# Kernel tuning notes

Hardware: AMD Instinct MI355X
Metric: run time of the kernel (lower is better)

The kernel has to match this reference:

```python
import jax, jax.numpy as jnp
import numpy as np

# Config constants (match init_kwargs)
THR = 0.2
TEMPERATURE = 0.1
BORDER_RM = 2
H0C, W0C = 60, 80  # L = 4800
H1C, W1C = 60, 80  # S = 4800


def setup_inputs() -> dict:
    key = jax.random.key(0)
    k0, k1 = jax.random.split(key)
    feat_c0 = jax.random.normal(k0, (2, 4800, 256), dtype=jnp.float32)
    feat_c1 = jax.random.normal(k1, (2, 4800, 256), dtype=jnp.float32)
    return {"feat_c0": feat_c0, "feat_c1": feat_c1}


def _border_mask_1d(h, w, b):
    """Flattened [h*w] bool mask that is False within b of any border."""
    ih = jnp.arange(h)
    iw = jnp.arange(w)
    mh = (ih >= b) & (ih < h - b)
    mw = (iw >= b) & (iw < w - b)
    return (mh[:, None] & mw[None, :]).reshape(-1)


def reference(feat_c0, feat_c1):
    N, L, C = feat_c0.shape
    # Normalize features and compute similarity (dual-softmax)
    scale = 1.0 / (C ** 0.5)
    sim = jnp.einsum('nlc,nsc->nls', feat_c0 * scale, feat_c1 * scale) / TEMPERATURE
    conf = jax.nn.softmax(sim, axis=1) * jax.nn.softmax(sim, axis=2)  # [N, L, S]

    # Threshold + border removal (mask_border path, no padding masks)
    bm0 = _border_mask_1d(H0C, W0C, BORDER_RM)  # [L]
    bm1 = _border_mask_1d(H1C, W1C, BORDER_RM)  # [S]
    mask = (conf > THR) & bm0[None, :, None] & bm1[None, None, :]

    # Mutual nearest neighbor
    mask = mask \
        & (conf == jnp.max(conf, axis=2, keepdims=True)) \
        & (conf == jnp.max(conf, axis=1, keepdims=True))

    # Per-row match: j index of the (at most one) surviving entry, and its conf.
    # Fixed-shape analogue of torch.where extraction: mconf==0 means no match.
    mask_v = jnp.any(mask, axis=2)                         # [N, L]
    j_ids = jnp.argmax(mask, axis=2)                       # [N, L]
    mconf = jnp.take_along_axis(conf, j_ids[..., None], axis=2)[..., 0]
    mconf = jnp.where(mask_v, mconf, 0.0)                  # [N, L]

    return conf, mask_v, j_ids, mconf
```

## Files before the change

kernel.cpp:

```cpp
#include <hip/hip_runtime.h>
#include <hip/hip_bf16.h>
#include <cstdint>

#define L_DIM 4800
#define C_DIM 256
#define CONF_ELEMS ((size_t)2 * L_DIM * L_DIM)

typedef _Float16 f16x8 __attribute__((ext_vector_type(8)));
typedef float f32x4 __attribute__((ext_vector_type(4)));

typedef const __attribute__((address_space(1))) uint32_t glb_u32;
typedef __attribute__((address_space(3))) uint32_t lds_u32;

#define WS_F16_NEEDED 15705600

__global__ __launch_bounds__(256) void k_cvt2(const float* __restrict__ f0,
                                              const float* __restrict__ f1,
                                              _Float16* __restrict__ h0,
                                              _Float16* __restrict__ h1) {
    int b = blockIdx.x;
    const float* src = (b < 1200) ? f0 : f1;
    _Float16* dst = (b < 1200) ? h0 : h1;
    int i = (b < 1200 ? b : b - 1200) * 256 + threadIdx.x;
    const float4* s4 = (const float4*)src;
    float4 a = s4[(size_t)i * 2], c = s4[(size_t)i * 2 + 1];
    f16x8 h = { (_Float16)a.x, (_Float16)a.y, (_Float16)a.z, (_Float16)a.w,
                (_Float16)c.x, (_Float16)c.y, (_Float16)c.z, (_Float16)c.w };
    *(f16x8*)(dst + (size_t)i * 8) = h;
}

__global__ __launch_bounds__(256) void k_reduceA(const float* __restrict__ partA,
                                                 float* __restrict__ invsum) {
    int i = blockIdx.x * 256 + threadIdx.x;
    if (i >= 19200) return;
    int base = (i < 9600) ? 0 : 50;
    int j = (i < 9600) ? i : i - 9600;
    float s = 0.f;
#pragma unroll 10
    for (int k = 0; k < 50; ++k)
        s += partA[(size_t)(base + k) * 9600 + j];
    invsum[i] = 1.0f / s;
}

__global__ __launch_bounds__(256) void k_reduceB(const unsigned* __restrict__ colbest,
                                                 unsigned* __restrict__ colmaxF) {
    int i = blockIdx.x * 256 + threadIdx.x;
    if (i >= 9600) return;
    unsigned m = 0u;
#pragma unroll 10
    for (int k = 0; k < 50; ++k)
        m = max(m, colbest[(size_t)k * 9600 + i]);
    colmaxF[i] = m;
}

template<bool F16SRC, bool FINAL>
__global__ __launch_bounds__(256) void k_gemm2(const void* __restrict__ srcA,
                                               const void* __restrict__ srcB,
                                               float* __restrict__ conf,
                                               const float* __restrict__ invsum,
                                               float* __restrict__ partA,
                                               unsigned long long* __restrict__ rowbest,
                                               unsigned* __restrict__ colbest) {
    const int xcd = blockIdx.x & 7;
    const int idx = blockIdx.x >> 3;
    const int t   = xcd * 625 + idx;
    const int n   = t / 2500;
    const int rem = t - n * 2500;
    const int ty  = rem / 50;
    const int tx  = rem - ty * 50;
    const int l0  = ty * 96;
    const int s0  = tx * 96;

    __shared__ __align__(16) _Float16 As[96 * 64];
    __shared__ __align__(16) _Float16 Bs[96 * 64];
    __shared__ __align__(16) char redbuf[2304];

    const int tid  = threadIdx.x;
    const int lane = tid & 63;
    const int w    = tid >> 6;
    const int wr   = w >> 1, wc = w & 1;
    const int q    = lane >> 4, r16 = lane & 15;

    f32x4 acc[3][3] = {};

    for (int kt = 0; kt < 4; ++kt) {
        const int k0 = kt * 64;
        __syncthreads();
        if constexpr (F16SRC) {
            const _Float16* A = (const _Float16*)srcA + ((size_t)n * L_DIM + l0) * C_DIM;
            const _Float16* B = (const _Float16*)srcB + ((size_t)n * L_DIM + s0) * C_DIM;
#pragma unroll
            for (int i = 0; i < 3; ++i) {
                int c   = tid + i * 256;
                int row = c >> 3;
                int kc  = (c & 7) ^ (row & 7);
                __builtin_amdgcn_global_load_lds(
                    (glb_u32*)(A + (size_t)row * C_DIM + k0 + kc * 8),
                    (lds_u32*)(As + (i * 256 + w * 64) * 8), 16, 0, 0);
                __builtin_amdgcn_global_load_lds(
                    (glb_u32*)(B + (size_t)row * C_DIM + k0 + kc * 8),
                    (lds_u32*)(Bs + (i * 256 + w * 64) * 8), 16, 0, 0);
            }
        } else {
            const float* A = (const float*)srcA + ((size_t)n * L_DIM + l0) * C_DIM;
            const float* B = (const float*)srcB + ((size_t)n * L_DIM + s0) * C_DIM;
#pragma unroll
            for (int i = 0; i < 3; ++i) {
                int c   = tid + i * 256;
                int row = c >> 3;
                int kc  = (c & 7) ^ (row & 7);
                const float* pa = A + (size_t)row * C_DIM + k0 + kc * 8;
                const float* pb = B + (size_t)row * C_DIM + k0 + kc * 8;
                float4 a0 = ((const float4*)pa)[0], a1 = ((const float4*)pa)[1];
                float4 b0 = ((const float4*)pb)[0], b1 = ((const float4*)pb)[1];
                f16x8 ha = { (_Float16)a0.x, (_Float16)a0.y, (_Float16)a0.z, (_Float16)a0.w,
                             (_Float16)a1.x, (_Float16)a1.y, (_Float16)a1.z, (_Float16)a1.w };
                f16x8 hb = { (_Float16)b0.x, (_Float16)b0.y, (_Float16)b0.z, (_Float16)b0.w,
                             (_Float16)b1.x, (_Float16)b1.y, (_Float16)b1.z, (_Float16)b1.w };
                *(f16x8*)(As + (size_t)c * 8) = ha;
                *(f16x8*)(Bs + (size_t)c * 8) = hb;
            }
        }
        __syncthreads();

        f16x8 af[2][3], bf[2][3];
#pragma unroll
        for (int m = 0; m < 3; ++m) {
            int row = wr * 48 + m * 16 + r16;
#pragma unroll
            for (int ks = 0; ks < 2; ++ks)
                af[ks][m] = *(const f16x8*)(As + row * 64 + (((ks * 4 + q) ^ (row & 7)) * 8));
        }
#pragma unroll
        for (int nn = 0; nn < 3; ++nn) {
            int row = wc * 48 + nn * 16 + r16;
#pragma unroll
            for (int ks = 0; ks < 2; ++ks)
                bf[ks][nn] = *(const f16x8*)(Bs + row * 64 + (((ks * 4 + q) ^ (row & 7)) * 8));
        }
#pragma unroll
        for (int ks = 0; ks < 2; ++ks)
#pragma unroll
            for (int m = 0; m < 3; ++m)
#pragma unroll
                for (int nn = 0; nn < 3; ++nn)
                    acc[m][nn] = __builtin_amdgcn_mfma_f32_16x16x32_f16(af[ks][m], bf[ks][nn], acc[m][nn], 0, 0, 0);
    }

    const float SIM_SCALE = 0.0390625f;

    if constexpr (!FINAL) {
        float* redR = (float*)redbuf;
        float* redC = (float*)(redbuf + 768);
        float cp[3] = {0.f, 0.f, 0.f};
#pragma unroll
        for (int m = 0; m < 3; ++m) {
#pragma unroll
            for (int reg = 0; reg < 4; ++reg) {
                float rsum = 0.f;
#pragma unroll
                for (int nn = 0; nn < 3; ++nn) {
                    float e = __expf(acc[m][nn][reg] * SIM_SCALE);
                    rsum += e;
                    cp[nn] += e;
                }
                rsum += __shfl_xor(rsum, 1);
                rsum += __shfl_xor(rsum, 2);
                rsum += __shfl_xor(rsum, 4);
                rsum += __shfl_xor(rsum, 8);
                if (r16 == 0)
                    redR[wc * 96 + wr * 48 + m * 16 + q * 4 + reg] = rsum;
            }
        }
#pragma unroll
        for (int nn = 0; nn < 3; ++nn) {
            float v = cp[nn];
            v += __shfl_xor(v, 16);
            v += __shfl_xor(v, 32);
            if (q == 0)
                redC[wr * 96 + wc * 48 + nn * 16 + r16] = v;
        }
        __syncthreads();
        if (tid < 96) {
            partA[(size_t)tx * 9600 + n * L_DIM + l0 + tid] = redR[tid] + redR[96 + tid];
        } else if (tid < 192) {
            int c = tid - 96;
            partA[(size_t)(50 + ty) * 9600 + n * L_DIM + s0 + c] = redC[c] + redC[96 + c];
        }
    } else {
        unsigned long long* redRB = (unsigned long long*)redbuf;
        unsigned* redCB = (unsigned*)(redbuf + 1536);
        const size_t base = (size_t)n * L_DIM * L_DIM;
        float ivC[3];
#pragma unroll
        for (int nn = 0; nn < 3; ++nn)
            ivC[nn] = invsum[9600 + n * L_DIM + s0 + wc * 48 + nn * 16 + r16];
        float cmx[3] = {0.f, 0.f, 0.f};
#pragma unroll
        for (int m = 0; m < 3; ++m) {
#pragma unroll
            for (int reg = 0; reg < 4; ++reg) {
                const int grow = l0 + wr * 48 + m * 16 + q * 4 + reg;
                const float ivR = invsum[n * L_DIM + grow];
                const size_t rowoff = base + (size_t)grow * L_DIM;
                float bv = -1.f; int bc = 0;
#pragma unroll
                for (int nn = 0; nn < 3; ++nn) {
                    const int gcol = s0 + wc * 48 + nn * 16 + r16;
                    float cf = __expf(acc[m][nn][reg] * (2.0f * SIM_SCALE)) * ivR * ivC[nn];
                    conf[rowoff + gcol] = cf;
                    cmx[nn] = fmaxf(cmx[nn], cf);
                    if (cf > bv) { bv = cf; bc = gcol; }
                }
                unsigned long long pack =
                    ((unsigned long long)__float_as_uint(bv) << 32) |
                    (unsigned long long)(0xFFFFFFFFu - (unsigned)bc);
#pragma unroll
                for (int d = 1; d < 16; d <<= 1) {
                    unsigned long long o = __shfl_xor(pack, d);
                    if (o > pack) pack = o;
                }
                if (r16 == 0)
                    redRB[wc * 96 + wr * 48 + m * 16 + q * 4 + reg] = pack;
            }
        }
#pragma unroll
        for (int nn = 0; nn < 3; ++nn) {
            float v = cmx[nn];
            v = fmaxf(v, __shfl_xor(v, 16));
            v = fmaxf(v, __shfl_xor(v, 32));
            if (q == 0)
                redCB[wr * 96 + wc * 48 + nn * 16 + r16] = __float_as_uint(v);
        }
        __syncthreads();
        if (tid < 96) {
            unsigned long long p0 = redRB[tid], p1 = redRB[96 + tid];
            rowbest[(size_t)tx * 9600 + n * L_DIM + l0 + tid] = (p0 > p1) ? p0 : p1;
        } else if (tid < 192) {
            int c = tid - 96;
            colbest[(size_t)ty * 9600 + n * L_DIM + s0 + c] = max(redCB[c], redCB[96 + c]);
        }
    }
}

__global__ __launch_bounds__(256) void k_match(const unsigned long long* __restrict__ rowbest,
                                               const unsigned* __restrict__ colmaxF,
                                               float* __restrict__ out) {
    int i = blockIdx.x * 256 + threadIdx.x;
    if (i >= 2 * L_DIM) return;
    unsigned long long p = 0ull;
#pragma unroll 10
    for (int k = 0; k < 50; ++k) {
        unsigned long long o = rowbest[(size_t)k * 9600 + i];
        if (o > p) p = o;
    }
    int n = i / L_DIM, l = i % L_DIM;
    float v = __uint_as_float((unsigned)(p >> 32));
    int cand = (int)(0xFFFFFFFFu - (unsigned)(p & 0xFFFFFFFFull));
    if (cand < 0 || cand >= L_DIM) cand = 0;
    int h0 = l / 80, w0 = l % 80;
    int h1 = cand / 80, w1 = cand % 80;
    bool bm0 = (h0 >= 2) && (h0 < 58) && (w0 >= 2) && (w0 < 78);
    bool bm1 = (h1 >= 2) && (h1 < 58) && (w1 >= 2) && (w1 < 78);
    float cm = __uint_as_float(colmaxF[n * L_DIM + cand]);
    bool mask = (v > 0.2f) && bm0 && bm1 && (v == cm);
    out[CONF_ELEMS + i]         = mask ? 1.0f : 0.0f;
    out[CONF_ELEMS + 9600 + i]  = mask ? (float)cand : 0.0f;
    out[CONF_ELEMS + 19200 + i] = mask ? v : 0.0f;
}

extern "C" void kernel_launch(void* const* d_in, const int* in_sizes, int n_in,
                              void* d_out, int out_size, void* d_ws, size_t ws_size,
                              hipStream_t stream) {
    const float* f0 = (const float*)d_in[0];
    const float* f1 = (const float*)d_in[1];
    float* out = (float*)d_out;

    float* invsum = (float*)d_ws;
    unsigned* colmaxF = (unsigned*)((char*)d_ws + 76800);
    float* partA = (float*)((char*)d_ws + 115200);
    unsigned long long* rowbest = (unsigned long long*)((char*)d_ws + 115200);
    unsigned* colbest = (unsigned*)((char*)d_ws + 3955200);
    _Float16* h0 = (_Float16*)((char*)d_ws + 5875200);
    _Float16* h1 = h0 + (size_t)2 * L_DIM * C_DIM;

    const bool usef16 = ws_size >= WS_F16_NEEDED;

    if (usef16) {
        k_cvt2<<<dim3(2400), 256, 0, stream>>>(f0, f1, h0, h1);
        k_gemm2<true, false><<<dim3(5000), 256, 0, stream>>>(
            h0, h1, out, invsum, partA, rowbest, colbest);
        k_reduceA<<<dim3(75), 256, 0, stream>>>(partA, invsum);
        k_gemm2<true, true><<<dim3(5000), 256, 0, stream>>>(
            h0, h1, out, invsum, partA, rowbest, colbest);
    } else {
        k_gemm2<false, false><<<dim3(5000), 256, 0, stream>>>(
            f0, f1, out, invsum, partA, rowbest, colbest);
        k_reduceA<<<dim3(75), 256, 0, stream>>>(partA, invsum);
        k_gemm2<false, true><<<dim3(5000), 256, 0, stream>>>(
            f0, f1, out, invsum, partA, rowbest, colbest);
    }
    k_reduceB<<<dim3(38), 256, 0, stream>>>(colbest, colmaxF);
    k_match<<<dim3(38), 256, 0, stream>>>(rowbest, colmaxF, out);
}
```

Before: 132.7 us.

## Double-buffer LDS tiles in dual-softmax GEMM to overlap loads with MFMA

```diff
diff --git a/kernel.cpp b/kernel.cpp
--- a/kernel.cpp
+++ b/kernel.cpp
@@ -71,8 +71,8 @@
     const int l0  = ty * 96;
     const int s0  = tx * 96;
 
-    __shared__ __align__(16) _Float16 As[96 * 64];
-    __shared__ __align__(16) _Float16 Bs[96 * 64];
+    __shared__ __align__(16) _Float16 As[2][96 * 64];
+    __shared__ __align__(16) _Float16 Bs[2][96 * 64];
     __shared__ __align__(16) char redbuf[2304];
 
     const int tid  = threadIdx.x;
@@ -83,60 +83,61 @@
 
     f32x4 acc[3][3] = {};
 
-    for (int kt = 0; kt < 4; ++kt) {
+    const _Float16* Ah = (const _Float16*)srcA + ((size_t)n * L_DIM + l0) * C_DIM;
+    const _Float16* Bh = (const _Float16*)srcB + ((size_t)n * L_DIM + s0) * C_DIM;
+    const float*    Af = (const float*)srcA + ((size_t)n * L_DIM + l0) * C_DIM;
+    const float*    Bf = (const float*)srcB + ((size_t)n * L_DIM + s0) * C_DIM;
+
+    auto stage = [&](int kt, int buf) {
         const int k0 = kt * 64;
-        __syncthreads();
         if constexpr (F16SRC) {
-            const _Float16* A = (const _Float16*)srcA + ((size_t)n * L_DIM + l0) * C_DIM;
-            const _Float16* B = (const _Float16*)srcB + ((size_t)n * L_DIM + s0) * C_DIM;
 #pragma unroll
             for (int i = 0; i < 3; ++i) {
                 int c   = tid + i * 256;
                 int row = c >> 3;
                 int kc  = (c & 7) ^ (row & 7);
                 __builtin_amdgcn_global_load_lds(
-                    (glb_u32*)(A + (size_t)row * C_DIM + k0 + kc * 8),
-                    (lds_u32*)(As + (i * 256 + w * 64) * 8), 16, 0, 0);
+                    (glb_u32*)(Ah + (size_t)row * C_DIM + k0 + kc * 8),
+                    (lds_u32*)(&As[buf][(i * 256 + w * 64) * 8]), 16, 0, 0);
                 __builtin_amdgcn_global_load_lds(
-                    (glb_u32*)(B + (size_t)row * C_DIM + k0 + kc * 8),
-                    (lds_u32*)(Bs + (i * 256 + w * 64) * 8), 16, 0, 0);
+                    (glb_u32*)(Bh + (size_t)row * C_DIM + k0 + kc * 8),
+                    (lds_u32*)(&Bs[buf][(i * 256 + w * 64) * 8]), 16, 0, 0);
             }
         } else {
-            const float* A = (const float*)srcA + ((size_t)n * L_DIM + l0) * C_DIM;
-            const float* B = (const float*)srcB + ((size_t)n * L_DIM + s0) * C_DIM;
 #pragma unroll
             for (int i = 0; i < 3; ++i) {
                 int c   = tid + i * 256;
                 int row = c >> 3;
                 int kc  = (c & 7) ^ (row & 7);
-                const float* pa = A + (size_t)row * C_DIM + k0 + kc * 8;
-                const float* pb = B + (size_t)row * C_DIM + k0 + kc * 8;
+                const float* pa = Af + (size_t)row * C_DIM + k0 + kc * 8;
+                const float* pb = Bf + (size_t)row * C_DIM + k0 + kc * 8;
                 float4 a0 = ((const float4*)pa)[0], a1 = ((const float4*)pa)[1];
                 float4 b0 = ((const float4*)pb)[0], b1 = ((const float4*)pb)[1];
                 f16x8 ha = { (_Float16)a0.x, (_Float16)a0.y, (_Float16)a0.z, (_Float16)a0.w,
                              (_Float16)a1.x, (_Float16)a1.y, (_Float16)a1.z, (_Float16)a1.w };
                 f16x8 hb = { (_Float16)b0.x, (_Float16)b0.y, (_Float16)b0.z, (_Float16)b0.w,
                              (_Float16)b1.x, (_Float16)b1.y, (_Float16)b1.z, (_Float16)b1.w };
-                *(f16x8*)(As + (size_t)c * 8) = ha;
-                *(f16x8*)(Bs + (size_t)c * 8) = hb;
+                *(f16x8*)(&As[buf][(size_t)c * 8]) = ha;
+                *(f16x8*)(&Bs[buf][(size_t)c * 8]) = hb;
             }
         }
-        __syncthreads();
-
+    };
+
+    auto compute = [&](int buf) {
         f16x8 af[2][3], bf[2][3];
 #pragma unroll
         for (int m = 0; m < 3; ++m) {
             int row = wr * 48 + m * 16 + r16;
 #pragma unroll
             for (int ks = 0; ks < 2; ++ks)
-                af[ks][m] = *(const f16x8*)(As + row * 64 + (((ks * 4 + q) ^ (row & 7)) * 8));
+                af[ks][m] = *(const f16x8*)(&As[buf][row * 64 + (((ks * 4 + q) ^ (row & 7)) * 8)]);
         }
 #pragma unroll
         for (int nn = 0; nn < 3; ++nn) {
             int row = wc * 48 + nn * 16 + r16;
 #pragma unroll
             for (int ks = 0; ks < 2; ++ks)
-                bf[ks][nn] = *(const f16x8*)(Bs + row * 64 + (((ks * 4 + q) ^ (row & 7)) * 8));
+                bf[ks][nn] = *(const f16x8*)(&Bs[buf][row * 64 + (((ks * 4 + q) ^ (row & 7)) * 8)]);
         }
 #pragma unroll
         for (int ks = 0; ks < 2; ++ks)
@@ -145,6 +146,15 @@
 #pragma unroll
                 for (int nn = 0; nn < 3; ++nn)
                     acc[m][nn] = __builtin_amdgcn_mfma_f32_16x16x32_f16(af[ks][m], bf[ks][nn], acc[m][nn], 0, 0, 0);
+    };
+
+    stage(0, 0);
+    __syncthreads();
+#pragma unroll
+    for (int kt = 0; kt < 4; ++kt) {
+        if (kt < 3) stage(kt + 1, (kt + 1) & 1);
+        compute(kt & 1);
+        __syncthreads();
     }
 
     const float SIM_SCALE = 0.0390625f;
```

Result: slower. 147.3 us (+11.0%).

## Loop five tiles per block, use nontemporal conf stores, fuse column-max reduce into match

Applied to the files above, without the earlier changes.

```diff
diff --git a/kernel.cpp b/kernel.cpp
--- a/kernel.cpp
+++ b/kernel.cpp
@@ -42,17 +42,6 @@
     invsum[i] = 1.0f / s;
 }
 
-__global__ __launch_bounds__(256) void k_reduceB(const unsigned* __restrict__ colbest,
-                                                 unsigned* __restrict__ colmaxF) {
-    int i = blockIdx.x * 256 + threadIdx.x;
-    if (i >= 9600) return;
-    unsigned m = 0u;
-#pragma unroll 10
-    for (int k = 0; k < 50; ++k)
-        m = max(m, colbest[(size_t)k * 9600 + i]);
-    colmaxF[i] = m;
-}
-
 template<bool F16SRC, bool FINAL>
 __global__ __launch_bounds__(256) void k_gemm2(const void* __restrict__ srcA,
                                                const void* __restrict__ srcB,
@@ -62,14 +51,7 @@
                                                unsigned long long* __restrict__ rowbest,
                                                unsigned* __restrict__ colbest) {
     const int xcd = blockIdx.x & 7;
-    const int idx = blockIdx.x >> 3;
-    const int t   = xcd * 625 + idx;
-    const int n   = t / 2500;
-    const int rem = t - n * 2500;
-    const int ty  = rem / 50;
-    const int tx  = rem - ty * 50;
-    const int l0  = ty * 96;
-    const int s0  = tx * 96;
+    const int j   = blockIdx.x >> 3;
 
     __shared__ __align__(16) _Float16 As[96 * 64];
     __shared__ __align__(16) _Float16 Bs[96 * 64];
@@ -81,170 +63,181 @@
     const int wr   = w >> 1, wc = w & 1;
     const int q    = lane >> 4, r16 = lane & 15;
 
-    f32x4 acc[3][3] = {};
-
-    for (int kt = 0; kt < 4; ++kt) {
-        const int k0 = kt * 64;
-        __syncthreads();
-        if constexpr (F16SRC) {
-            const _Float16* A = (const _Float16*)srcA + ((size_t)n * L_DIM + l0) * C_DIM;
-            const _Float16* B = (const _Float16*)srcB + ((size_t)n * L_DIM + s0) * C_DIM;
-#pragma unroll
-            for (int i = 0; i < 3; ++i) {
-                int c   = tid + i * 256;
-                int row = c >> 3;
-                int kc  = (c & 7) ^ (row & 7);
-                __builtin_amdgcn_global_load_lds(
-                    (glb_u32*)(A + (size_t)row * C_DIM + k0 + kc * 8),
-                    (lds_u32*)(As + (i * 256 + w * 64) * 8), 16, 0, 0);
-                __builtin_amdgcn_global_load_lds(
-                    (glb_u32*)(B + (size_t)row * C_DIM + k0 + kc * 8),
-                    (lds_u32*)(Bs + (i * 256 + w * 64) * 8), 16, 0, 0);
+    const float SIM_SCALE = 0.0390625f;
+
+    for (int s = 0; s < 5; ++s) {
+        const int t   = xcd * 625 + j + s * 125;
+        const int n   = t / 2500;
+        const int rem = t - n * 2500;
+        const int ty  = rem / 50;
+        const int tx  = rem - ty * 50;
+        const int l0  = ty * 96;
+        const int s0  = tx * 96;
+
+        f32x4 acc[3][3] = {};
+
+        const _Float16* Ah = (const _Float16*)srcA + ((size_t)n * L_DIM + l0) * C_DIM;
+        const _Float16* Bh = (const _Float16*)srcB + ((size_t)n * L_DIM + s0) * C_DIM;
+        const float*    Af = (const float*)srcA + ((size_t)n * L_DIM + l0) * C_DIM;
+        const float*    Bf = (const float*)srcB + ((size_t)n * L_DIM + s0) * C_DIM;
+
+        for (int kt = 0; kt < 4; ++kt) {
+            const int k0 = kt * 64;
+            __syncthreads();
+            if constexpr (F16SRC) {
+#pragma unroll
+                for (int i = 0; i < 3; ++i) {
+                    int c   = tid + i * 256;
+                    int row = c >> 3;
+                    int kc  = (c & 7) ^ (row & 7);
+                    __builtin_amdgcn_global_load_lds(
+                        (glb_u32*)(Ah + (size_t)row * C_DIM + k0 + kc * 8),
+                        (lds_u32*)(As + (i * 256 + w * 64) * 8), 16, 0, 0);
+                    __builtin_amdgcn_global_load_lds(
+                        (glb_u32*)(Bh + (size_t)row * C_DIM + k0 + kc * 8),
+                        (lds_u32*)(Bs + (i * 256 + w * 64) * 8), 16, 0, 0);
+                }
+            } else {
+#pragma unroll
+                for (int i = 0; i < 3; ++i) {
+                    int c   = tid + i * 256;
+                    int row = c >> 3;
+                    int kc  = (c & 7) ^ (row & 7);
+                    const float* pa = Af + (size_t)row * C_DIM + k0 + kc * 8;
+                    const float* pb = Bf + (size_t)row * C_DIM + k0 + kc * 8;
+                    float4 a0 = ((const float4*)pa)[0], a1 = ((const float4*)pa)[1];
+                    float4 b0 = ((const float4*)pb)[0], b1 = ((const float4*)pb)[1];
+                    f16x8 ha = { (_Float16)a0.x, (_Float16)a0.y, (_Float16)a0.z, (_Float16)a0.w,
+                                 (_Float16)a1.x, (_Float16)a1.y, (_Float16)a1.z, (_Float16)a1.w };
+                    f16x8 hb = { (_Float16)b0.x, (_Float16)b0.y, (_Float16)b0.z, (_Float16)b0.w,
+                                 (_Float16)b1.x, (_Float16)b1.y, (_Float16)b1.z, (_Float16)b1.w };
+                    *(f16x8*)(As + (size_t)c * 8) = ha;
+                    *(f16x8*)(Bs + (size_t)c * 8) = hb;
+                }
+            }
+            __syncthreads();
+
+            f16x8 af[2][3], bf[2][3];
+#pragma unroll
+            for (int m = 0; m < 3; ++m) {
+                int row = wr * 48 + m * 16 + r16;
+#pragma unroll
+                for (int ks = 0; ks < 2; ++ks)
+                    af[ks][m] = *(const f16x8*)(As + row * 64 + (((ks * 4 + q) ^ (row & 7)) * 8));
+            }
+#pragma unroll
+            for (int nn = 0; nn < 3; ++nn) {
+                int row = wc * 48 + nn * 16 + r16;
+#pragma unroll
+                for (int ks = 0; ks < 2; ++ks)
+                    bf[ks][nn] = *(const f16x8*)(Bs + row * 64 + (((ks * 4 + q) ^ (row & 7)) * 8));
+            }
+#pragma unroll
+            for (int ks = 0; ks < 2; ++ks)
+#pragma unroll
+                for (int m = 0; m < 3; ++m)
+#pragma unroll
+                    for (int nn = 0; nn < 3; ++nn)
+                        acc[m][nn] = __builtin_amdgcn_mfma_f32_16x16x32_f16(af[ks][m], bf[ks][nn], acc[m][nn], 0, 0, 0);
+        }
+
+        if constexpr (!FINAL) {
+            float* redR = (float*)redbuf;
+            float* redC = (float*)(redbuf + 768);
+            float cp[3] = {0.f, 0.f, 0.f};
+#pragma unroll
+            for (int m = 0; m < 3; ++m) {
+#pragma unroll
+                for (int reg = 0; reg < 4; ++reg) {
+                    float rsum = 0.f;
+#pragma unroll
+                    for (int nn = 0; nn < 3; ++nn) {
+                        float e = __expf(acc[m][nn][reg] * SIM_SCALE);
+                        rsum += e;
+                        cp[nn] += e;
+                    }
+                    rsum += __shfl_xor(rsum, 1);
+                    rsum += __shfl_xor(rsum, 2);
+                    rsum += __shfl_xor(rsum, 4);
+                    rsum += __shfl_xor(rsum, 8);
+                    if (r16 == 0)
+                        redR[wc * 96 + wr * 48 + m * 16 + q * 4 + reg] = rsum;
+                }
+            }
+#pragma unroll
+            for (int nn = 0; nn < 3; ++nn) {
+                float v = cp[nn];
+                v += __shfl_xor(v, 16);
+                v += __shfl_xor(v, 32);
+                if (q == 0)
+                    redC[wr * 96 + wc * 48 + nn * 16 + r16] = v;
+            }
+            __syncthreads();
+            if (tid < 96) {
+                partA[(size_t)tx * 9600 + n * L_DIM + l0 + tid] = redR[tid] + redR[96 + tid];
+            } else if (tid < 192) {
+                int c = tid - 96;
+                partA[(size_t)(50 + ty) * 9600 + n * L_DIM + s0 + c] = redC[c] + redC[96 + c];
             }
         } else {
-            const float* A = (const float*)srcA + ((size_t)n * L_DIM + l0) * C_DIM;
-            const float* B = (const float*)srcB + ((size_t)n * L_DIM + s0) * C_DIM;
-#pragma unroll
-            for (int i = 0; i < 3; ++i) {
-                int c   = tid + i * 256;
-                int row = c >> 3;
-                int kc  = (c & 7) ^ (row & 7);
-                const float* pa = A + (size_t)row * C_DIM + k0 + kc * 8;
-                const float* pb = B + (size_t)row * C_DIM + k0 + kc * 8;
-                float4 a0 = ((const float4*)pa)[0], a1 = ((const float4*)pa)[1];
-                float4 b0 = ((const float4*)pb)[0], b1 = ((const float4*)pb)[1];
-                f16x8 ha = { (_Float16)a0.x, (_Float16)a0.y, (_Float16)a0.z, (_Float16)a0.w,
-                             (_Float16)a1.x, (_Float16)a1.y, (_Float16)a1.z, (_Float16)a1.w };
-                f16x8 hb = { (_Float16)b0.x, (_Float16)b0.y, (_Float16)b0.z, (_Float16)b0.w,
-                             (_Float16)b1.x, (_Float16)b1.y, (_Float16)b1.z, (_Float16)b1.w };
-                *(f16x8*)(As + (size_t)c * 8) = ha;
-                *(f16x8*)(Bs + (size_t)c * 8) = hb;
-            }
-        }
-        __syncthreads();
-
-        f16x8 af[2][3], bf[2][3];
-#pragma unroll
-        for (int m = 0; m < 3; ++m) {
-            int row = wr * 48 + m * 16 + r16;
-#pragma unroll
-            for (int ks = 0; ks < 2; ++ks)
-                af[ks][m] = *(const f16x8*)(As + row * 64 + (((ks * 4 + q) ^ (row & 7)) * 8));
-        }
-#pragma unroll
-        for (int nn = 0; nn < 3; ++nn) {
-            int row = wc * 48 + nn * 16 + r16;
-#pragma unroll
-            for (int ks = 0; ks < 2; ++ks)
-                bf[ks][nn] = *(const f16x8*)(Bs + row * 64 + (((ks * 4 + q) ^ (row & 7)) * 8));
-        }
-#pragma unroll
-        for (int ks = 0; ks < 2; ++ks)
-#pragma unroll
-            for (int m = 0; m < 3; ++m)
-#pragma unroll
-                for (int nn = 0; nn < 3; ++nn)
-                    acc[m][nn] = __builtin_amdgcn_mfma_f32_16x16x32_f16(af[ks][m], bf[ks][nn], acc[m][nn], 0, 0, 0);
-    }
-
-    const float SIM_SCALE = 0.0390625f;
-
-    if constexpr (!FINAL) {
-        float* redR = (float*)redbuf;
-        float* redC = (float*)(redbuf + 768);
-        float cp[3] = {0.f, 0.f, 0.f};
-#pragma unroll
-        for (int m = 0; m < 3; ++m) {
-#pragma unroll
-            for (int reg = 0; reg < 4; ++reg) {
-                float rsum = 0.f;
-#pragma unroll
-                for (int nn = 0; nn < 3; ++nn) {
-                    float e = __expf(acc[m][nn][reg] * SIM_SCALE);
-                    rsum += e;
-                    cp[nn] += e;
+            unsigned long long* redRB = (unsigned long long*)redbuf;
+            unsigned* redCB = (unsigned*)(redbuf + 1536);
+            const size_t base = (size_t)n * L_DIM * L_DIM;
+            float ivC[3];
+#pragma unroll
+            for (int nn = 0; nn < 3; ++nn)
+                ivC[nn] = invsum[9600 + n * L_DIM + s0 + wc * 48 + nn * 16 + r16];
+            float cmx[3] = {0.f, 0.f, 0.f};
+#pragma unroll
+            for (int m = 0; m < 3; ++m) {
+#pragma unroll
+                for (int reg = 0; reg < 4; ++reg) {
+                    const int grow = l0 + wr * 48 + m * 16 + q * 4 + reg;
+                    const float ivR = invsum[n * L_DIM + grow];
+                    const size_t rowoff = base + (size_t)grow * L_DIM;
+                    float bv = -1.f; int bc = 0;
+#pragma unroll
+                    for (int nn = 0; nn < 3; ++nn) {
+                        const int gcol = s0 + wc * 48 + nn * 16 + r16;
+                        float cf = __expf(acc[m][nn][reg] * (2.0f * SIM_SCALE)) * ivR * ivC[nn];
+                        __builtin_nontemporal_store(cf, &conf[rowoff + gcol]);
+                        cmx[nn] = fmaxf(cmx[nn], cf);
+                        if (cf > bv) { bv = cf; bc = gcol; }
+                    }
+                    unsigned long long pack =
+                        ((unsigned long long)__float_as_uint(bv) << 32) |
+                        (unsigned long long)(0xFFFFFFFFu - (unsigned)bc);
+#pragma unroll
+                    for (int d = 1; d < 16; d <<= 1) {
+                        unsigned long long o = __shfl_xor(pack, d);
+                        if (o > pack) pack = o;
+                    }
+                    if (r16 == 0)
+                        redRB[wc * 96 + wr * 48 + m * 16 + q * 4 + reg] = pack;
                 }
-                rsum += __shfl_xor(rsum, 1);
-                rsum += __shfl_xor(rsum, 2);
-                rsum += __shfl_xor(rsum, 4);
-                rsum += __shfl_xor(rsum, 8);
-                if (r16 == 0)
-                    redR[wc * 96 + wr * 48 + m * 16 + q * 4 + reg] = rsum;
-            }
-        }
-#pragma unroll
-        for (int nn = 0; nn < 3; ++nn) {
-            float v = cp[nn];
-            v += __shfl_xor(v, 16);
-            v += __shfl_xor(v, 32);
-            if (q == 0)
-                redC[wr * 96 + wc * 48 + nn * 16 + r16] = v;
-        }
-        __syncthreads();
-        if (tid < 96) {
-            partA[(size_t)tx * 9600 + n * L_DIM + l0 + tid] = redR[tid] + redR[96 + tid];
-        } else if (tid < 192) {
-            int c = tid - 96;
-            partA[(size_t)(50 + ty) * 9600 + n * L_DIM + s0 + c] = redC[c] + redC[96 + c];
-        }
-    } else {
-        unsigned long long* redRB = (unsigned long long*)redbuf;
-        unsigned* redCB = (unsigned*)(redbuf + 1536);
-        const size_t base = (size_t)n * L_DIM * L_DIM;
-        float ivC[3];
-#pragma unroll
-        for (int nn = 0; nn < 3; ++nn)
-            ivC[nn] = invsum[9600 + n * L_DIM + s0 + wc * 48 + nn * 16 + r16];
-        float cmx[3] = {0.f, 0.f, 0.f};
-#pragma unroll
-        for (int m = 0; m < 3; ++m) {
-#pragma unroll
-            for (int reg = 0; reg < 4; ++reg) {
-                const int grow = l0 + wr * 48 + m * 16 + q * 4 + reg;
-                const float ivR = invsum[n * L_DIM + grow];
-                const size_t rowoff = base + (size_t)grow * L_DIM;
-                float bv = -1.f; int bc = 0;
-#pragma unroll
-                for (int nn = 0; nn < 3; ++nn) {
-                    const int gcol = s0 + wc * 48 + nn * 16 + r16;
-                    float cf = __expf(acc[m][nn][reg] * (2.0f * SIM_SCALE)) * ivR * ivC[nn];
-                    conf[rowoff + gcol] = cf;
-                    cmx[nn] = fmaxf(cmx[nn], cf);
-                    if (cf > bv) { bv = cf; bc = gcol; }
-                }
-                unsigned long long pack =
-                    ((unsigned long long)__float_as_uint(bv) << 32) |
-                    (unsigned long long)(0xFFFFFFFFu - (unsigned)bc);
-#pragma unroll
-                for (int d = 1; d < 16; d <<= 1) {
-                    unsigned long long o = __shfl_xor(pack, d);
-                    if (o > pack) pack = o;
-                }
-                if (r16 == 0)
-                    redRB[wc * 96 + wr * 48 + m * 16 + q * 4 + reg] = pack;
-            }
-        }
-#pragma unroll
-        for (int nn = 0; nn < 3; ++nn) {
-            float v = cmx[nn];
-            v = fmaxf(v, __shfl_xor(v, 16));
-            v = fmaxf(v, __shfl_xor(v, 32));
-            if (q == 0)
-                redCB[wr * 96 + wc * 48 + nn * 16 + r16] = __float_as_uint(v);
-        }
-        __syncthreads();
-        if (tid < 96) {
-            unsigned long long p0 = redRB[tid], p1 = redRB[96 + tid];
-            rowbest[(size_t)tx * 9600 + n * L_DIM + l0 + tid] = (p0 > p1) ? p0 : p1;
-        } else if (tid < 192) {
-            int c = tid - 96;
-            colbest[(size_t)ty * 9600 + n * L_DIM + s0 + c] = max(redCB[c], redCB[96 + c]);
+            }
+#pragma unroll
+            for (int nn = 0; nn < 3; ++nn) {
+                float v = cmx[nn];
+                v = fmaxf(v, __shfl_xor(v, 16));
+                v = fmaxf(v, __shfl_xor(v, 32));
+                if (q == 0)
+                    redCB[wr * 96 + wc * 48 + nn * 16 + r16] = __float_as_uint(v);
+            }
+            __syncthreads();
+            if (tid < 96) {
+                unsigned long long p0 = redRB[tid], p1 = redRB[96 + tid];
+                rowbest[(size_t)tx * 9600 + n * L_DIM + l0 + tid] = (p0 > p1) ? p0 : p1;
+            } else if (tid < 192) {
+                int c = tid - 96;
+                colbest[(size_t)ty * 9600 + n * L_DIM + s0 + c] = max(redCB[c], redCB[96 + c]);
+            }
         }
     }
 }
 
 __global__ __launch_bounds__(256) void k_match(const unsigned long long* __restrict__ rowbest,
-                                               const unsigned* __restrict__ colmaxF,
+                                               const unsigned* __restrict__ colbest,
                                                float* __restrict__ out) {
     int i = blockIdx.x * 256 + threadIdx.x;
     if (i >= 2 * L_DIM) return;
@@ -258,11 +251,15 @@
     float v = __uint_as_float((unsigned)(p >> 32));
     int cand = (int)(0xFFFFFFFFu - (unsigned)(p & 0xFFFFFFFFull));
     if (cand < 0 || cand >= L_DIM) cand = 0;
+    unsigned cmu = 0u;
+#pragma unroll 10
+    for (int k = 0; k < 50; ++k)
+        cmu = max(cmu, colbest[(size_t)k * 9600 + n * L_DIM + cand]);
     int h0 = l / 80, w0 = l % 80;
     int h1 = cand / 80, w1 = cand % 80;
     bool bm0 = (h0 >= 2) && (h0 < 58) && (w0 >= 2) && (w0 < 78);
     bool bm1 = (h1 >= 2) && (h1 < 58) && (w1 >= 2) && (w1 < 78);
-    float cm = __uint_as_float(colmaxF[n * L_DIM + cand]);
+    float cm = __uint_as_float(cmu);
     bool mask = (v > 0.2f) && bm0 && bm1 && (v == cm);
     out[CONF_ELEMS + i]         = mask ? 1.0f : 0.0f;
     out[CONF_ELEMS + 9600 + i]  = mask ? (float)cand : 0.0f;
@@ -277,7 +274,6 @@
     float* out = (float*)d_out;
 
     float* invsum = (float*)d_ws;
-    unsigned* colmaxF = (unsigned*)((char*)d_ws + 76800);
     float* partA = (float*)((char*)d_ws + 115200);
     unsigned long long* rowbest = (unsigned long long*)((char*)d_ws + 115200);
     unsigned* colbest = (unsigned*)((char*)d_ws + 3955200);
@@ -288,18 +284,17 @@
 
     if (usef16) {
         k_cvt2<<<dim3(2400), 256, 0, stream>>>(f0, f1, h0, h1);
-        k_gemm2<true, false><<<dim3(5000), 256, 0, stream>>>(
+        k_gemm2<true, false><<<dim3(1000), 256, 0, stream>>>(
             h0, h1, out, invsum, partA, rowbest, colbest);
         k_reduceA<<<dim3(75), 256, 0, stream>>>(partA, invsum);
-        k_gemm2<true, true><<<dim3(5000), 256, 0, stream>>>(
+        k_gemm2<true, true><<<dim3(1000), 256, 0, stream>>>(
             h0, h1, out, invsum, partA, rowbest, colbest);
     } else {
-        k_gemm2<false, false><<<dim3(5000), 256, 0, stream>>>(
+        k_gemm2<false, false><<<dim3(1000), 256, 0, stream>>>(
             f0, f1, out, invsum, partA, rowbest, colbest);
         k_reduceA<<<dim3(75), 256, 0, stream>>>(partA, invsum);
-        k_gemm2<false, true><<<dim3(5000), 256, 0, stream>>>(
+        k_gemm2<false, true><<<dim3(1000), 256, 0, stream>>>(
             f0, f1, out, invsum, partA, rowbest, colbest);
     }
-    k_reduceB<<<dim3(38), 256, 0, stream>>>(colbest, colmaxF);
-    k_match<<<dim3(38), 256, 0, stream>>>(rowbest, colmaxF, out);
-}
+    k_match<<<dim3(38), 256, 0, stream>>>(rowbest, colbest, out);
+}
```

After: 157.0 us. 18.3% more time.
